# Performance work log

Measured on AMD Instinct MI355X. Metric: run time of the kernel, lower is better.

Reference implementation:

```python
import jax, jax.numpy as jnp
import numpy as np

N = 50000
E = 1600000
IN_DIM = 64
EMB_DIM = 64
DENSE = 128
HEADS = 2
GATD = 64
SLOPE = 0.2


def gat_conv(x, src, dst, W, al, ar, b):
    # DGL GATConv: x [N, Fin], W [Fin, H*D], al/ar/b [H, D]
    n = x.shape[0]
    H, D = al.shape
    z = (x @ W).reshape(n, H, D)                      # [N,H,D]
    el = jnp.sum(z * al, axis=-1)                     # [N,H]
    er = jnp.sum(z * ar, axis=-1)                     # [N,H]
    e = jax.nn.leaky_relu(el[src] + er[dst], SLOPE)   # [E,H]
    # edge softmax grouped by destination node
    m = jax.ops.segment_max(e, dst, num_segments=n)   # [N,H]
    ex = jnp.exp(e - m[dst])                          # [E,H]
    s = jax.ops.segment_sum(ex, dst, num_segments=n)  # [N,H]
    alpha = ex / s[dst]                               # [E,H]
    out = jax.ops.segment_sum(alpha[:, :, None] * z[src], dst, num_segments=n)
    return out + b                                    # [N,H,D]


def setup_inputs() -> dict:
    key = jax.random.key(0)
    ks = jax.random.split(key, 20)
    g = lambda k, sh: jax.random.normal(k, sh, dtype=jnp.float32) * 0.05
    inp = {
        "feat": jax.random.normal(ks[0], (N, IN_DIM), dtype=jnp.float32),
        "node_ids": jax.random.randint(ks[1], (N,), 0, N, dtype=jnp.int32),
        "src": jax.random.randint(ks[2], (E,), 0, N, dtype=jnp.int32),
        "dst": jax.random.randint(ks[3], (E,), 0, N, dtype=jnp.int32),
        "emb": g(ks[4], (N, EMB_DIM)),
        "dense_w": g(ks[5], (IN_DIM + EMB_DIM, DENSE)),
        "dense_b": jnp.zeros((DENSE,), jnp.float32),
        "g1_w": g(ks[6], (DENSE, HEADS * GATD)),
        "g1_al": g(ks[7], (HEADS, GATD)),
        "g1_ar": g(ks[8], (HEADS, GATD)),
        "g1_b": jnp.zeros((HEADS, GATD), jnp.float32),
        "g2_w": g(ks[9], (HEADS * GATD, HEADS * GATD)),
        "g2_al": g(ks[10], (HEADS, GATD)),
        "g2_ar": g(ks[11], (HEADS, GATD)),
        "g2_b": jnp.zeros((HEADS, GATD), jnp.float32),
        "out_w": g(ks[12], (HEADS * GATD, 1)),
        "out_al": g(ks[13], (1, 1)),
        "out_ar": g(ks[14], (1, 1)),
        "out_b": jnp.zeros((1, 1), jnp.float32),
    }
    return inp


def reference(feat, node_ids, src, dst, emb, dense_w, dense_b,
              g1_w, g1_al, g1_ar, g1_b, g2_w, g2_al, g2_ar, g2_b,
              out_w, out_al, out_ar, out_b):
    # embedding concat + initial dense + ReLU
    h = jnp.concatenate([emb[node_ids], feat], axis=-1)   # [N, 128]
    h = jax.nn.relu(h @ dense_w + dense_b)                # [N, 128]
    # GAT layer 1: ReLU then concat heads (reshape N, H*D)
    h = jax.nn.relu(gat_conv(h, src, dst, g1_w, g1_al, g1_ar, g1_b))
    h = h.reshape(h.shape[0], -1)                         # [N, H*D]
    # GAT layer 2
    h = jax.nn.relu(gat_conv(h, src, dst, g2_w, g2_al, g2_ar, g2_b))
    h = h.reshape(h.shape[0], -1)
    # output GAT layer, 1 head, squeeze head dim
    h = gat_conv(h, src, dst, out_w, out_al, out_ar, out_b)  # [N,1,1]
    return h[:, 0, :]                                        # [N,1]
```

## Files before the change

kernel.cpp:

```cpp
#include <hip/hip_runtime.h>
#include <cfloat>
#include <cmath>


#define CBG 256
#define CAPC 12288
#define TILE 8192
#define BIMG 10240

typedef __attribute__((ext_vector_type(8))) short short8v;
typedef __attribute__((ext_vector_type(4))) float f32x4;

__device__ __forceinline__ float lrelu(float x) { return x > 0.f ? x : 0.2f * x; }

__device__ __forceinline__ uint32_t bf16_rne(float f) {
  uint32_t u = __float_as_uint(f);
  return (u + 0x7fffu + ((u >> 16) & 1u)) >> 16;
}
__device__ __forceinline__ uint32_t pack_hilo(float v) {
  uint32_t h = bf16_rne(v);
  float r = v - __uint_as_float(h << 16);
  return (h << 16) | bf16_rne(r);
}

__global__ __launch_bounds__(256) void bucketA_kernel(
    const int* __restrict__ src, const int* __restrict__ dst,
    int* __restrict__ scount, uint32_t* __restrict__ tmp, int e, int ncb) {
  __shared__ int cnt[256];
  __shared__ int lscan[256];
  __shared__ int gbase[256];
  __shared__ uint32_t image[TILE];
  const int t = threadIdx.x;
  const int e0 = blockIdx.x * TILE;
  const int ne = min(TILE, e - e0);

  for (int i = t; i < 256; i += 256) cnt[i] = 0;
  __syncthreads();
  for (int i = t; i < ne; i += 256) atomicAdd(&cnt[dst[e0 + i] >> 8], 1);
  __syncthreads();
  if (t < 64) {
    int carry = 0;
    for (int base = 0; base < ncb; base += 64) {
      int idx = base + t;
      int c = (idx < ncb) ? cnt[idx] : 0;
      int v = c;
#pragma unroll
      for (int off = 1; off < 64; off <<= 1) {
        int u = __shfl_up(v, off, 64);
        if (t >= off) v += u;
      }
      if (idx < ncb) lscan[idx] = carry + v - c;
      carry += __shfl(v, 63, 64);
    }
  }
  __syncthreads();
  for (int b = t; b < ncb; b += 256)
    gbase[b] = (cnt[b] > 0) ? atomicAdd(&scount[b], cnt[b]) : 0;
  __syncthreads();
  for (int b = t; b < ncb; b += 256) cnt[b] = 0;
  __syncthreads();
  for (int i = t; i < ne; i += 256) {
    int d = dst[e0 + i], s = src[e0 + i];
    int b = d >> 8;
    int r = atomicAdd(&cnt[b], 1);
    image[lscan[b] + r] =
        (uint32_t)s | ((uint32_t)(d & 255) << 16) | ((uint32_t)b << 24);
  }
  __syncthreads();
  for (int j = t; j < ne; j += 256) {
    uint32_t w = image[j];
    int b = w >> 24;
    int pos = gbase[b] + (j - lscan[b]);
    if (pos < CAPC) tmp[(size_t)b * CAPC + pos] = w & 0xFFFFFFu;
  }
}

__global__ __launch_bounds__(256) void bucketB_kernel(
    const uint32_t* __restrict__ tmp, const int* __restrict__ scount,
    int* __restrict__ row_start, int* __restrict__ csr_src, int n, int ncb, int e) {
  __shared__ int cnt[256];
  __shared__ int cur[256];
  __shared__ int wsum[4];
  __shared__ int s_base;
  __shared__ uint32_t image[BIMG];
  const int b = blockIdx.x, t = threadIdx.x, lane = t & 63, wid = t >> 6;

  if (t < 64) {
    int part = 0;
    for (int idx = lane; idx < b; idx += 64) part += scount[idx];
#pragma unroll
    for (int off = 32; off; off >>= 1) part += __shfl_xor(part, off, 64);
    if (lane == 0) s_base = part;
  }
  cnt[t] = 0;
  __syncthreads();
  const int total = min(scount[b], CAPC);
  const int base = s_base;
  const uint32_t* strm = tmp + (size_t)b * CAPC;

  for (int i = t; i < total; i += 256) atomicAdd(&cnt[(strm[i] >> 16) & 255], 1);
  __syncthreads();
  int c = cnt[t], v = c;
#pragma unroll
  for (int off = 1; off < 64; off <<= 1) {
    int u = __shfl_up(v, off, 64);
    if (lane >= off) v += u;
  }
  if (lane == 63) wsum[wid] = v;
  __syncthreads();
  if (t == 0) {
    int acc = 0;
#pragma unroll
    for (int w = 0; w < 4; w++) { int x = wsum[w]; wsum[w] = acc; acc += x; }
  }
  __syncthreads();
  int ex = wsum[wid] + v - c;
  cur[t] = ex;
  int d = b * CBG + t;
  if (d < n) row_start[d] = base + ex;
  if (b == 0 && t == 0) row_start[n] = e;
  __syncthreads();
  for (int i = t; i < total; i += 256) {
    uint32_t w = strm[i];
    int dl = (w >> 16) & 255;
    int pos = atomicAdd(&cur[dl], 1);
    if (pos < BIMG) image[pos] = w & 0xFFFFu;
    else csr_src[base + pos] = (int)(w & 0xFFFFu);
  }
  __syncthreads();
  const int lim = total < BIMG ? total : BIMG;
  for (int j = t; j < lim; j += 256) csr_src[base + j] = (int)image[j];
}

__global__ void hist_kernel(const int* __restrict__ dst, int* __restrict__ cnt, int e) {
  for (int i = blockIdx.x * blockDim.x + threadIdx.x; i < e; i += gridDim.x * blockDim.x)
    atomicAdd(&cnt[dst[i]], 1);
}
__global__ void scatter_kernel(const int* __restrict__ src, const int* __restrict__ dst,
                               const int* __restrict__ row_start, int* __restrict__ cursor,
                               int* __restrict__ csr_src, int e) {
  for (int i = blockIdx.x * blockDim.x + threadIdx.x; i < e; i += gridDim.x * blockDim.x) {
    int d = dst[i];
    int pos = atomicAdd(&cursor[d], 1);
    csr_src[row_start[d] + pos] = src[i];
  }
}
__global__ __launch_bounds__(1024) void scan1_kernel(const int* __restrict__ cnt,
                                                     int* __restrict__ row_start,
                                                     int* __restrict__ bsum, int n) {
  __shared__ int wsum[16];
  const int t = threadIdx.x, lane = t & 63, wid = t >> 6;
  int i = blockIdx.x * 1024 + t;
  int c = (i < n) ? cnt[i] : 0;
  int v = c;
#pragma unroll
  for (int off = 1; off < 64; off <<= 1) {
    int u = __shfl_up(v, off, 64);
    if (lane >= off) v += u;
  }
  if (lane == 63) wsum[wid] = v;
  __syncthreads();
  if (t == 0) {
    int acc = 0;
#pragma unroll
    for (int w = 0; w < 16; w++) { int x = wsum[w]; wsum[w] = acc; acc += x; }
    bsum[blockIdx.x] = acc;
  }
  __syncthreads();
  if (i < n) row_start[i] = wsum[wid] + v - c;
}
__global__ __launch_bounds__(64) void scan2_kernel(int* __restrict__ bsum, int nb) {
  const int lane = threadIdx.x;
  int carry = 0;
  for (int base = 0; base < nb; base += 64) {
    int idx = base + lane;
    int c = (idx < nb) ? bsum[idx] : 0;
    int v = c;
#pragma unroll
    for (int off = 1; off < 64; off <<= 1) {
      int u = __shfl_up(v, off, 64);
      if (lane >= off) v += u;
    }
    if (idx < nb) bsum[idx] = carry + v - c;
    carry += __shfl(v, 63, 64);
  }
}
__global__ void scan3_kernel(int* __restrict__ row_start, const int* __restrict__ bsum,
                             int n, int e) {
  int i = blockIdx.x * blockDim.x + threadIdx.x;
  if (i < n) row_start[i] += bsum[i >> 10];
  if (i == 0) row_start[n] = e;
}

__global__ __launch_bounds__(256) void wswz3_kernel(
    const float* __restrict__ W0, const float* __restrict__ W1,
    const float* __restrict__ W2, short* __restrict__ Whi0,
    short* __restrict__ Wlo0, short* __restrict__ Whi1, short* __restrict__ Wlo1,
    short* __restrict__ Whi2, short* __restrict__ Wlo2) {
  int which = blockIdx.x >> 3;
  const float* W = which == 0 ? W0 : (which == 1 ? W1 : W2);
  short* Whi = which == 0 ? Whi0 : (which == 1 ? Whi1 : Whi2);
  short* Wlo = which == 0 ? Wlo0 : (which == 1 ? Wlo1 : Wlo2);
  int fid = (blockIdx.x & 7) * 256 + threadIdx.x;
  int lane = fid & 63;
  int cq = fid >> 6;
  int q = cq >> 3, c = cq & 7;
  int col = c * 16 + (lane & 15);
  int k0 = q * 32 + (lane >> 4) * 8;
#pragma unroll
  for (int j = 0; j < 8; j++) {
    float v = W[(k0 + j) * 128 + col];
    uint32_t h = bf16_rne(v);
    float r = v - __uint_as_float(h << 16);
    Whi[fid * 8 + j] = (short)h;
    Wlo[fid * 8 + j] = (short)bf16_rne(r);
  }
}

template <int MODE>
__global__ __launch_bounds__(256) void mfmm_kernel(
    const uint32_t* __restrict__ Xp, const short* __restrict__ Whi,
    const short* __restrict__ Wlo, const float* __restrict__ bias,
    uint32_t* __restrict__ Hp, uint32_t* __restrict__ zp,
    float2* __restrict__ el2, float2* __restrict__ er2,
    const float* __restrict__ al, const float* __restrict__ ar, int n,
    const float* __restrict__ emb, const int* __restrict__ ids,
    const float* __restrict__ feat) {
  __shared__ short Ahi[64 * 136];
  __shared__ short Alo[64 * 136];
  const int t = threadIdx.x;
  const int nb = blockIdx.x * 64;

  for (int idx = t; idx < 64 * 32; idx += 256) {
    int nl = idx >> 5, k4 = (idx & 31) << 2;
    int node = nb + nl;
    uint32_t h01 = 0, h23 = 0, l01 = 0, l23 = 0;
    if (node < n) {
      if (MODE == 1) {
        uint4 w = *(const uint4*)&Xp[(size_t)node * 128 + k4];
        h01 = (w.x >> 16) | (w.y & 0xffff0000u);
        l01 = (w.x & 0xffffu) | (w.y << 16);
        h23 = (w.z >> 16) | (w.w & 0xffff0000u);
        l23 = (w.z & 0xffffu) | (w.w << 16);
      } else {
        float4 v;
        if (k4 < 64) v = *(const float4*)&emb[(size_t)ids[node] * 64 + k4];
        else         v = *(const float4*)&feat[(size_t)node * 64 + (k4 - 64)];
        uint32_t a0 = bf16_rne(v.x), a1 = bf16_rne(v.y);
        uint32_t a2 = bf16_rne(v.z), a3 = bf16_rne(v.w);
        h01 = a0 | (a1 << 16);
        h23 = a2 | (a3 << 16);
        l01 = bf16_rne(v.x - __uint_as_float(a0 << 16)) |
              (bf16_rne(v.y - __uint_as_float(a1 << 16)) << 16);
        l23 = bf16_rne(v.z - __uint_as_float(a2 << 16)) |
              (bf16_rne(v.w - __uint_as_float(a3 << 16)) << 16);
      }
    }
    *(uint2*)&Ahi[nl * 136 + k4] = make_uint2(h01, h23);
    *(uint2*)&Alo[nl * 136 + k4] = make_uint2(l01, l23);
  }
  __syncthreads();

  const int lane = t & 63, wv = t >> 6;
  const int r16 = lane & 15, g = lane >> 4;
  const int arow = (wv * 16 + r16) * 136;

  f32x4 acc[8];
#pragma unroll
  for (int c = 0; c < 8; c++) acc[c] = (f32x4){0.f, 0.f, 0.f, 0.f};

#pragma unroll
  for (int q = 0; q < 4; q++) {
    int ka = q * 32 + g * 8;
    short8v ahi = *(const short8v*)&Ahi[arow + ka];
    short8v alo = *(const short8v*)&Alo[arow + ka];
#pragma unroll
    for (int c = 0; c < 8; c++) {
      short8v bhi = *(const short8v*)&Whi[(((q * 8 + c) * 64) + lane) * 8];
      short8v blo = *(const short8v*)&Wlo[(((q * 8 + c) * 64) + lane) * 8];
      acc[c] = __builtin_amdgcn_mfma_f32_16x16x32_bf16(ahi, bhi, acc[c], 0, 0, 0);
      acc[c] = __builtin_amdgcn_mfma_f32_16x16x32_bf16(ahi, blo, acc[c], 0, 0, 0);
      acc[c] = __builtin_amdgcn_mfma_f32_16x16x32_bf16(alo, bhi, acc[c], 0, 0, 0);
    }
  }

  const int node_base = nb + wv * 16;
  if (MODE == 0) {
#pragma unroll
    for (int c = 0; c < 8; c++) {
      int col = c * 16 + r16;
      float bv = bias[col];
#pragma unroll
      for (int r = 0; r < 4; r++) {
        int node = node_base + g * 4 + r;
        if (node < n) {
          float v = fmaxf(acc[c][r] + bv, 0.f);
          Hp[(size_t)node * 128 + col] = pack_hilo(v);
        }
      }
    }
  } else {
    float p0l[4] = {0, 0, 0, 0}, p1l[4] = {0, 0, 0, 0};
    float p0r[4] = {0, 0, 0, 0}, p1r[4] = {0, 0, 0, 0};
#pragma unroll
    for (int c = 0; c < 8; c++) {
      int col = c * 16 + r16;
      float av = al[col], rv = ar[col];
#pragma unroll
      for (int r = 0; r < 4; r++) {
        if (c < 4) { p0l[r] = fmaf(acc[c][r], av, p0l[r]); p0r[r] = fmaf(acc[c][r], rv, p0r[r]); }
        else       { p1l[r] = fmaf(acc[c][r], av, p1l[r]); p1r[r] = fmaf(acc[c][r], rv, p1r[r]); }
      }
    }
#pragma unroll
    for (int c = 0; c < 8; c++) {
#pragma unroll
      for (int r = 0; r < 4; r++) {
        float other = __shfl_xor(acc[c][r], 1, 64);
        int node = node_base + g * 4 + r;
        if (!(lane & 1) && node < n) {
          uint32_t w = bf16_rne(acc[c][r]) | (bf16_rne(other) << 16);
          zp[(size_t)node * 64 + c * 8 + (r16 >> 1)] = w;
        }
      }
    }
#pragma unroll
    for (int off = 1; off < 16; off <<= 1) {
#pragma unroll
      for (int r = 0; r < 4; r++) {
        p0l[r] += __shfl_xor(p0l[r], off, 64);
        p1l[r] += __shfl_xor(p1l[r], off, 64);
        p0r[r] += __shfl_xor(p0r[r], off, 64);
        p1r[r] += __shfl_xor(p1r[r], off, 64);
      }
    }
    if (r16 == 0) {
#pragma unroll
      for (int r = 0; r < 4; r++) {
        int node = node_base + g * 4 + r;
        if (node < n) {
          el2[node] = make_float2(p0l[r], p1l[r]);
          er2[node] = make_float2(p0r[r], p1r[r]);
        }
      }
    }
  }
}

#define CAP 256
__global__ __launch_bounds__(256) void agg12_kernel(
    const uint32_t* __restrict__ zp, const float2* __restrict__ el2,
    const float2* __restrict__ er2, const int* __restrict__ row_start,
    const int* __restrict__ csr_src, const float* __restrict__ bias,
    uint32_t* __restrict__ Hp,
    const float* __restrict__ ow, const float* __restrict__ oal,
    const float* __restrict__ oar, float* __restrict__ z3,
    float* __restrict__ el3, float* __restrict__ er3, int n, int fuse_out) {
  __shared__ float ecf[4][2][CAP];
  __shared__ int sc[4][CAP];
  const int w = threadIdx.x >> 6, lane = threadIdx.x & 63;
  const int hl = lane >> 5, l32 = lane & 31;
  const int node = blockIdx.x * 4 + w;
  const bool valid = node < n;
  int rs = 0, deg = 0;
  float er_h = 0.f;
  if (valid) {
    rs = row_start[node];
    deg = row_start[node + 1] - rs;
    er_h = ((const float*)&er2[node])[hl];
  }
  const int cdeg = deg < CAP ? deg : CAP;

  float sp_h = 0.f;
  for (int i = l32; i < deg; i += 32) {
    int s = csr_src[rs + i];
    float lv = ((const float*)&el2[s])[hl];
    float x = __expf(lrelu(lv + er_h));
    if (i < CAP) {
      if (hl == 0) sc[w][i] = s;
      ecf[w][hl][i] = x;
    }
    sp_h += x;
  }
#pragma unroll
  for (int off = 16; off; off >>= 1) sp_h += __shfl_xor(sp_h, off, 64);
  __syncthreads();

  const float* exh = ecf[w][hl];
  float ae = 0.f, ao = 0.f;
  int i = 0;
  for (; i + 16 <= cdeg; i += 16) {
    int s16[16];
    float x16[16];
#pragma unroll
    for (int q = 0; q < 4; q++) {
      int4 s4 = *(const int4*)&sc[w][i + q * 4];
      float4 x4 = *(const float4*)&exh[i + q * 4];
      s16[q * 4 + 0] = s4.x; s16[q * 4 + 1] = s4.y;
      s16[q * 4 + 2] = s4.z; s16[q * 4 + 3] = s4.w;
      x16[q * 4 + 0] = x4.x; x16[q * 4 + 1] = x4.y;
      x16[q * 4 + 2] = x4.z; x16[q * 4 + 3] = x4.w;
    }
    uint32_t zw[16];
#pragma unroll
    for (int u = 0; u < 16; u++) zw[u] = zp[(size_t)s16[u] * 64 + lane];
#pragma unroll
    for (int u = 0; u < 16; u++) {
      ae = fmaf(x16[u], __uint_as_float(zw[u] << 16), ae);
      ao = fmaf(x16[u], __uint_as_float(zw[u] & 0xffff0000u), ao);
    }
  }
  for (; i + 4 <= cdeg; i += 4) {
    int4 s4 = *(const int4*)&sc[w][i];
    float4 x4 = *(const float4*)&exh[i];
    uint32_t z0 = zp[(size_t)s4.x * 64 + lane];
    uint32_t z1 = zp[(size_t)s4.y * 64 + lane];
    uint32_t z2 = zp[(size_t)s4.z * 64 + lane];
    uint32_t z3v = zp[(size_t)s4.w * 64 + lane];
    ae = fmaf(x4.x, __uint_as_float(z0 << 16), ae);
    ao = fmaf(x4.x, __uint_as_float(z0 & 0xffff0000u), ao);
    ae = fmaf(x4.y, __uint_as_float(z1 << 16), ae);
    ao = fmaf(x4.y, __uint_as_float(z1 & 0xffff0000u), ao);
    ae = fmaf(x4.z, __uint_as_float(z2 << 16), ae);
    ao = fmaf(x4.z, __uint_as_float(z2 & 0xffff0000u), ao);
    ae = fmaf(x4.w, __uint_as_float(z3v << 16), ae);
    ao = fmaf(x4.w, __uint_as_float(z3v & 0xffff0000u), ao);
  }
  for (; i < cdeg; i++) {
    int s = sc[w][i];
    float x = exh[i];
    uint32_t zw = zp[(size_t)s * 64 + lane];
    ae = fmaf(x, __uint_as_float(zw << 16), ae);
    ao = fmaf(x, __uint_as_float(zw & 0xffff0000u), ao);
  }
  for (; i < deg; i++) {
    int s = csr_src[rs + i];
    float x = __expf(lrelu(((const float*)&el2[s])[hl] + er_h));
    uint32_t zw = zp[(size_t)s * 64 + lane];
    ae = fmaf(x, __uint_as_float(zw << 16), ae);
    ao = fmaf(x, __uint_as_float(zw & 0xffff0000u), ao);
  }

  if (valid) {
    float2 b2 = reinterpret_cast<const float2*>(bias)[lane];
    float oe, oo;
    if (deg == 0) { oe = b2.x; oo = b2.y; }
    else { oe = ae / sp_h + b2.x; oo = ao / sp_h + b2.y; }
    oe = fmaxf(oe, 0.f);
    oo = fmaxf(oo, 0.f);
    if (!fuse_out) {
      *(uint2*)&Hp[(size_t)node * 128 + 2 * lane] =
          make_uint2(pack_hilo(oe), pack_hilo(oo));
    } else {
      float2 w2 = reinterpret_cast<const float2*>(ow)[lane];
      float d = oe * w2.x + oo * w2.y;
#pragma unroll
      for (int off = 32; off; off >>= 1) d += __shfl_xor(d, off, 64);
      if (lane == 0) {
        z3[node] = d;
        el3[node] = d * oal[0];
        er3[node] = d * oar[0];
      }
    }
  }
}

__global__ __launch_bounds__(256) void agg3_kernel(
    const float* __restrict__ z3, const float* __restrict__ el3,
    const float* __restrict__ er3, const int* __restrict__ row_start,
    const int* __restrict__ csr_src, const float* __restrict__ b,
    float* __restrict__ out, int n) {
  int node = blockIdx.x * 8 + (threadIdx.x >> 5);
  int l32 = threadIdx.x & 31;
  if (node >= n) return;
  int rs = row_start[node];
  int deg = row_start[node + 1] - rs;
  float er = er3[node];
  float sp = 0.f, ap = 0.f;
  for (int i = l32; i < deg; i += 32) {
    int s = csr_src[rs + i];
    float ex = __expf(lrelu(el3[s] + er));
    sp += ex;
    ap = fmaf(ex, z3[s], ap);
  }
#pragma unroll
  for (int off = 16; off; off >>= 1) {
    sp += __shfl_xor(sp, off, 64);
    ap += __shfl_xor(ap, off, 64);
  }
  if (l32 == 0) out[node] = (deg == 0) ? b[0] : (ap / sp + b[0]);
}

extern "C" void kernel_launch(void* const* d_in, const int* in_sizes, int n_in,
                              void* d_out, int out_size, void* d_ws, size_t ws_size,
                              hipStream_t stream) {
  const float* feat     = (const float*)d_in[0];
  const int*   node_ids = (const int*)d_in[1];
  const int*   src      = (const int*)d_in[2];
  const int*   dst      = (const int*)d_in[3];
  const float* emb      = (const float*)d_in[4];
  const float* dense_w  = (const float*)d_in[5];
  const float* dense_b  = (const float*)d_in[6];
  const float* g1_w     = (const float*)d_in[7];
  const float* g1_al    = (const float*)d_in[8];
  const float* g1_ar    = (const float*)d_in[9];
  const float* g1_b     = (const float*)d_in[10];
  const float* g2_w     = (const float*)d_in[11];
  const float* g2_al    = (const float*)d_in[12];
  const float* g2_ar    = (const float*)d_in[13];
  const float* g2_b     = (const float*)d_in[14];
  const float* out_w    = (const float*)d_in[15];
  const float* out_al   = (const float*)d_in[16];
  const float* out_ar   = (const float*)d_in[17];
  const float* out_b    = (const float*)d_in[18];
  const int n = in_sizes[0] / 64;
  const int e = in_sizes[2];

  const int ncb = (n + CBG - 1) / CBG;

  char* ws = (char*)d_ws;
  size_t off = 0;
  auto alloc = [&](size_t bytes) -> void* {
    void* p = ws + off;
    off += (bytes + 255) & ~(size_t)255;
    return p;
  };
  uint32_t* Hp       = (uint32_t*)alloc((size_t)n * 128 * 4);
  size_t zp_bytes    = (size_t)n * 64 * 4;
  size_t tmp_bytes   = (size_t)ncb * CAPC * 4;
  uint32_t* zp       = (uint32_t*)alloc(zp_bytes > tmp_bytes ? zp_bytes : tmp_bytes);
  uint32_t* tmp      = zp;
  float2*   el2      = (float2*)alloc((size_t)n * 8);
  float2*   er2      = (float2*)alloc((size_t)n * 8);
  float*    z3       = (float*)alloc((size_t)n * 4);
  float*    el3      = (float*)alloc((size_t)n * 4);
  float*    er3      = (float*)alloc((size_t)n * 4);
  int*      scount   = (int*)alloc((size_t)ncb * 4);
  int*      row_start= (int*)alloc((size_t)(n + 1) * 4);
  int*      csr_src  = (int*)alloc((size_t)e * 4);
  short*    Wd_hi    = (short*)alloc(2048 * 8 * 2);
  short*    Wd_lo    = (short*)alloc(2048 * 8 * 2);
  short*    W1_hi    = (short*)alloc(2048 * 8 * 2);
  short*    W1_lo    = (short*)alloc(2048 * 8 * 2);
  short*    W2_hi    = (short*)alloc(2048 * 8 * 2);
  short*    W2_lo    = (short*)alloc(2048 * 8 * 2);
  int*      cnt      = (int*)alloc((size_t)n * 4);
  int*      cursor   = (int*)alloc((size_t)n * 4);
  const int nblk     = (n + 1023) / 1024;
  int*      bsum     = (int*)alloc((size_t)nblk * 4);

  wswz3_kernel<<<24, 256, 0, stream>>>(dense_w, g1_w, g2_w,
                                       Wd_hi, Wd_lo, W1_hi, W1_lo, W2_hi, W2_lo);

  if (n < 65536) {
    hipMemsetAsync(scount, 0, (size_t)ncb * 4, stream);
    const int natile = (e + TILE - 1) / TILE;
    bucketA_kernel<<<natile, 256, 0, stream>>>(src, dst, scount, tmp, e, ncb);
    bucketB_kernel<<<ncb, 256, 0, stream>>>(tmp, scount, row_start, csr_src,
                                            n, ncb, e);
  } else {
    hipMemsetAsync(cnt, 0, (size_t)n * 4, stream);
    hipMemsetAsync(cursor, 0, (size_t)n * 4, stream);
    hist_kernel<<<2048, 256, 0, stream>>>(dst, cnt, e);
    scan1_kernel<<<nblk, 1024, 0, stream>>>(cnt, row_start, bsum, n);
    scan2_kernel<<<1, 64, 0, stream>>>(bsum, nblk);
    scan3_kernel<<<(n + 255) / 256, 256, 0, stream>>>(row_start, bsum, n, e);
    scatter_kernel<<<2048, 256, 0, stream>>>(src, dst, row_start, cursor, csr_src, e);
  }

  const int mmgrid = (n + 63) / 64;
  const int ngrid4 = (n + 3) / 4;
  const int ngrid8 = (n + 7) / 8;

  mfmm_kernel<0><<<mmgrid, 256, 0, stream>>>(nullptr, Wd_hi, Wd_lo, dense_b,
                                             Hp, nullptr, nullptr, nullptr,
                                             nullptr, nullptr, n, emb, node_ids, feat);
  mfmm_kernel<1><<<mmgrid, 256, 0, stream>>>(Hp, W1_hi, W1_lo, nullptr,
                                             nullptr, zp, el2, er2,
                                             g1_al, g1_ar, n, nullptr, nullptr, nullptr);
  agg12_kernel<<<ngrid4, 256, 0, stream>>>(zp, el2, er2, row_start, csr_src, g1_b, Hp,
                                           nullptr, nullptr, nullptr, nullptr, nullptr,
                                           nullptr, n, 0);
  mfmm_kernel<1><<<mmgrid, 256, 0, stream>>>(Hp, W2_hi, W2_lo, nullptr,
                                             nullptr, zp, el2, er2,
                                             g2_al, g2_ar, n, nullptr, nullptr, nullptr);
  agg12_kernel<<<ngrid4, 256, 0, stream>>>(zp, el2, er2, row_start, csr_src, g2_b, nullptr,
                                           out_w, out_al, out_ar, z3, el3, er3, n, 1);
  agg3_kernel<<<ngrid8, 256, 0, stream>>>(z3, el3, er3, row_start, csr_src, out_b,
                                          (float*)d_out, n);
}
```

Measured before the change: 265.9 us.

## Compute both heads per lane in GAT aggregation and shrink edge tile

The aggregation kernel now has each of the 64 lanes compute edge scores for both heads, covering 64 edges per pass instead of 32, and stores them as float2 pairs in shared memory. The gather loop is cut from 16-wide to 8-wide unrolling, with per-lane head selection, and the softmax sums are reduced across the full wavefront. Separately, the TILE constant is halved. Together these change register pressure, shared-memory access patterns and memory-level parallelism in the gather loop, with mixed effects on latency hiding.

```diff
diff --git a/kernel.cpp b/kernel.cpp
--- a/kernel.cpp
+++ b/kernel.cpp
@@ -5,7 +5,7 @@
 
 #define CBG 256
 #define CAPC 12288
-#define TILE 8192
+#define TILE 4096
 #define BIMG 10240
 
 typedef __attribute__((ext_vector_type(8))) short short8v;
@@ -356,96 +356,80 @@
     const float* __restrict__ ow, const float* __restrict__ oal,
     const float* __restrict__ oar, float* __restrict__ z3,
     float* __restrict__ el3, float* __restrict__ er3, int n, int fuse_out) {
-  __shared__ float ecf[4][2][CAP];
+  __shared__ float2 ec[4][CAP];
   __shared__ int sc[4][CAP];
   const int w = threadIdx.x >> 6, lane = threadIdx.x & 63;
-  const int hl = lane >> 5, l32 = lane & 31;
   const int node = blockIdx.x * 4 + w;
   const bool valid = node < n;
   int rs = 0, deg = 0;
-  float er_h = 0.f;
+  float er0 = 0.f, er1 = 0.f;
   if (valid) {
     rs = row_start[node];
     deg = row_start[node + 1] - rs;
-    er_h = ((const float*)&er2[node])[hl];
+    float2 e2 = er2[node];
+    er0 = e2.x; er1 = e2.y;
   }
   const int cdeg = deg < CAP ? deg : CAP;
 
-  float sp_h = 0.f;
-  for (int i = l32; i < deg; i += 32) {
+  float sp0 = 0.f, sp1 = 0.f;
+  for (int i = lane; i < deg; i += 64) {
     int s = csr_src[rs + i];
-    float lv = ((const float*)&el2[s])[hl];
-    float x = __expf(lrelu(lv + er_h));
-    if (i < CAP) {
-      if (hl == 0) sc[w][i] = s;
-      ecf[w][hl][i] = x;
-    }
-    sp_h += x;
-  }
-#pragma unroll
-  for (int off = 16; off; off >>= 1) sp_h += __shfl_xor(sp_h, off, 64);
-  __syncthreads();
-
-  const float* exh = ecf[w][hl];
+    float2 l = el2[s];
+    float x0 = __expf(lrelu(l.x + er0));
+    float x1 = __expf(lrelu(l.y + er1));
+    if (i < CAP) { sc[w][i] = s; ec[w][i] = make_float2(x0, x1); }
+    sp0 += x0; sp1 += x1;
+  }
+#pragma unroll
+  for (int off = 32; off; off >>= 1) {
+    sp0 += __shfl_xor(sp0, off, 64);
+    sp1 += __shfl_xor(sp1, off, 64);
+  }
+  __syncthreads();
+
   float ae = 0.f, ao = 0.f;
   int i = 0;
-  for (; i + 16 <= cdeg; i += 16) {
-    int s16[16];
-    float x16[16];
-#pragma unroll
-    for (int q = 0; q < 4; q++) {
-      int4 s4 = *(const int4*)&sc[w][i + q * 4];
-      float4 x4 = *(const float4*)&exh[i + q * 4];
-      s16[q * 4 + 0] = s4.x; s16[q * 4 + 1] = s4.y;
-      s16[q * 4 + 2] = s4.z; s16[q * 4 + 3] = s4.w;
-      x16[q * 4 + 0] = x4.x; x16[q * 4 + 1] = x4.y;
-      x16[q * 4 + 2] = x4.z; x16[q * 4 + 3] = x4.w;
-    }
-    uint32_t zw[16];
-#pragma unroll
-    for (int u = 0; u < 16; u++) zw[u] = zp[(size_t)s16[u] * 64 + lane];
-#pragma unroll
-    for (int u = 0; u < 16; u++) {
-      ae = fmaf(x16[u], __uint_as_float(zw[u] << 16), ae);
-      ao = fmaf(x16[u], __uint_as_float(zw[u] & 0xffff0000u), ao);
-    }
-  }
-  for (; i + 4 <= cdeg; i += 4) {
-    int4 s4 = *(const int4*)&sc[w][i];
-    float4 x4 = *(const float4*)&exh[i];
-    uint32_t z0 = zp[(size_t)s4.x * 64 + lane];
-    uint32_t z1 = zp[(size_t)s4.y * 64 + lane];
-    uint32_t z2 = zp[(size_t)s4.z * 64 + lane];
-    uint32_t z3v = zp[(size_t)s4.w * 64 + lane];
-    ae = fmaf(x4.x, __uint_as_float(z0 << 16), ae);
-    ao = fmaf(x4.x, __uint_as_float(z0 & 0xffff0000u), ao);
-    ae = fmaf(x4.y, __uint_as_float(z1 << 16), ae);
-    ao = fmaf(x4.y, __uint_as_float(z1 & 0xffff0000u), ao);
-    ae = fmaf(x4.z, __uint_as_float(z2 << 16), ae);
-    ao = fmaf(x4.z, __uint_as_float(z2 & 0xffff0000u), ao);
-    ae = fmaf(x4.w, __uint_as_float(z3v << 16), ae);
-    ao = fmaf(x4.w, __uint_as_float(z3v & 0xffff0000u), ao);
+  for (; i + 8 <= cdeg; i += 8) {
+    uint32_t zw[8];
+    float xh[8];
+#pragma unroll
+    for (int u = 0; u < 8; u++) {
+      int s = sc[w][i + u];
+      float2 ex = ec[w][i + u];
+      xh[u] = (lane < 32) ? ex.x : ex.y;
+      zw[u] = zp[(size_t)s * 64 + lane];
+    }
+#pragma unroll
+    for (int u = 0; u < 8; u++) {
+      ae = fmaf(xh[u], __uint_as_float(zw[u] << 16), ae);
+      ao = fmaf(xh[u], __uint_as_float(zw[u] & 0xffff0000u), ao);
+    }
   }
   for (; i < cdeg; i++) {
     int s = sc[w][i];
-    float x = exh[i];
+    float2 ex = ec[w][i];
+    float x = (lane < 32) ? ex.x : ex.y;
     uint32_t zw = zp[(size_t)s * 64 + lane];
     ae = fmaf(x, __uint_as_float(zw << 16), ae);
     ao = fmaf(x, __uint_as_float(zw & 0xffff0000u), ao);
   }
   for (; i < deg; i++) {
     int s = csr_src[rs + i];
-    float x = __expf(lrelu(((const float*)&el2[s])[hl] + er_h));
+    float2 l = el2[s];
+    float x0 = __expf(lrelu(l.x + er0));
+    float x1 = __expf(lrelu(l.y + er1));
+    float x = (lane < 32) ? x0 : x1;
     uint32_t zw = zp[(size_t)s * 64 + lane];
     ae = fmaf(x, __uint_as_float(zw << 16), ae);
     ao = fmaf(x, __uint_as_float(zw & 0xffff0000u), ao);
   }
 
   if (valid) {
+    float sp = (lane < 32) ? sp0 : sp1;
     float2 b2 = reinterpret_cast<const float2*>(bias)[lane];
     float oe, oo;
     if (deg == 0) { oe = b2.x; oo = b2.y; }
-    else { oe = ae / sp_h + b2.x; oo = ao / sp_h + b2.y; }
+    else { oe = ae / sp + b2.x; oo = ao / sp + b2.y; }
     oe = fmaxf(oe, 0.f);
     oo = fmaxf(oo, 0.f);
     if (!fuse_out) {
```

Measured after the change: 240.3 us. 1.11x faster.
